# Kernel optimization log

Hardware: AMD Instinct MI355X
Metric: run time of the kernel (lower is better)

## Reference

```python
import jax, jax.numpy as jnp
import numpy as np

TEXT_H = 4096
VISION_H = 1024
SPATIAL_SCALE = 4
DIM = VISION_H * SPATIAL_SCALE  # 4096
B, S, P = 2, 4096, 1024


def setup_inputs() -> dict:
    key = jax.random.key(0)
    ks = jax.random.split(key, 6)
    x = jax.random.normal(ks[0], (B, S, TEXT_H), dtype=jnp.float32)
    total_mask = jax.random.randint(ks[1], (B, S), 0, 2).astype(bool)
    prefix_mask = jnp.ones((B, P), dtype=bool)
    # MLP params: Linear(text->text), GELU, Linear(text->vision*scale)
    W1 = jax.random.normal(ks[2], (TEXT_H, TEXT_H), dtype=jnp.float32) / np.sqrt(TEXT_H)
    b1 = jnp.zeros((TEXT_H,), dtype=jnp.float32)
    W2 = jax.random.normal(ks[3], (TEXT_H, DIM), dtype=jnp.float32) / np.sqrt(TEXT_H)
    b2 = jnp.zeros((DIM,), dtype=jnp.float32)
    return {"x": x, "total_mask": total_mask, "prefix_mask": prefix_mask,
            "W1": W1, "b1": b1, "W2": W2, "b2": b2}


def reference(x, total_mask, prefix_mask, W1, b1, W2, b2):
    # out = zeros; out[total_mask] = mlp(x[total_mask])
    # Equivalent dense form (jit-friendly, same math on every output element):
    h = jax.nn.gelu(jnp.einsum('bst,th->bsh', x, W1) + b1, approximate=False)
    y = jnp.einsum('bsh,hd->bsd', h, W2) + b2          # [B, S, DIM]
    out = jnp.where(total_mask[:, :, None], y, jnp.zeros((), dtype=y.dtype))
    out = out.reshape(out.shape[0], -1, VISION_H)      # [B, S*SCALE, VISION_H]
    prefix_len = prefix_mask.shape[1] * SPATIAL_SCALE  # use_perceiver == False path
    return out[:, prefix_len:]                         # [B, S*SCALE - prefix_len, VISION_H]
```

## Files before the change

kernel.cpp:

```cpp
#include <hip/hip_runtime.h>
#include <hip/hip_bf16.h>
#include <cstdint>
#include <cstddef>

#define TEXT_H_   4096
#define S_TOK     4096
#define P_TOK     1024
#define ROWS_PB   3072
#define M_ROWS    6144
#define NK        4096
#define BK        64
#define NT        (NK / BK)

#define BM0       256
#define BN        256
#define NWGC      384
#define SLOT0_BYTES (64 * 1024)
#define LDS0_TOTAL  (2 * SLOT0_BYTES)

typedef __attribute__((ext_vector_type(8))) short  bf16x8_t;
typedef __attribute__((ext_vector_type(4))) float  f32x4_t;
typedef __attribute__((ext_vector_type(4))) float  fl4_t;
typedef __attribute__((ext_vector_type(4))) ushort u16x4_t;
typedef __attribute__((ext_vector_type(8))) ushort u16x8_t;

__device__ int g_meff;
__device__ int g_rowmap[M_ROWS];

__device__ __forceinline__ ushort f2bf(float f) {
  uint32_t u = __float_as_uint(f);
  u += 0x7FFFu + ((u >> 16) & 1u);
  return (ushort)(u >> 16);
}

__device__ __forceinline__ void gload_lds16(const void* g, void* l) {
  __builtin_amdgcn_global_load_lds((const __attribute__((address_space(1))) void*)g,
                                   (__attribute__((address_space(3))) void*)l, 16, 0, 0);
}

#define BARRIER()    asm volatile("s_barrier" ::: "memory")
#define WAIT_LGKM(n) asm volatile("s_waitcnt lgkmcnt(" #n ")" ::: "memory")
#define WAIT_VM(n)   asm volatile("s_waitcnt vmcnt(" #n ")" ::: "memory")

__global__ void scan_mask_kernel(const void* __restrict__ mask) {
  __shared__ int cnt[1024];
  const int t = threadIdx.x;
  const unsigned* mw = (const unsigned*)mask;
  int isbool = 0;
  for (int i = 0; i < 64; ++i)
    if (mw[i] & ~1u) isbool = 1;
  int pred[6]; int c = 0;
#pragma unroll
  for (int j = 0; j < 6; ++j) {
    const int m  = t * 6 + j;
    const int bb = (m >= ROWS_PB) ? 1 : 0;
    const int idx = bb * S_TOK + P_TOK + (m - bb * ROWS_PB);
    const int v = isbool ? (int)((const unsigned char*)mask)[idx]
                         : ((const int*)mask)[idx];
    pred[j] = (v != 0);
    c += pred[j];
  }
  cnt[t] = c;
  __syncthreads();
  for (int off = 1; off < 1024; off <<= 1) {
    const int v = (t >= off) ? cnt[t - off] : 0;
    __syncthreads();
    cnt[t] += v;
    __syncthreads();
  }
  int p = cnt[t] - c;
  if (t == 1023) g_meff = cnt[1023];
#pragma unroll
  for (int j = 0; j < 6; ++j) {
    const int m = t * 6 + j;
    if (pred[j]) g_rowmap[p++] = m;
  }
}

__global__ void convert_xc_kernel(const float* __restrict__ x, ushort* __restrict__ A1) {
  const int i = blockIdx.x;
  if (i >= g_meff) return;
  const int m  = g_rowmap[i];
  const int bb = (m >= ROWS_PB) ? 1 : 0;
  const int s  = P_TOK + (m - bb * ROWS_PB);
  const float* src = x + ((size_t)bb * S_TOK + s) * TEXT_H_;
  ushort* dst = A1 + (size_t)i * TEXT_H_;
  const int t = threadIdx.x;
#pragma unroll
  for (int c = 0; c < 2; ++c) {
    const int base = t * 16 + c * 8;
    fl4_t f0 = *(const fl4_t*)(src + base);
    fl4_t f1 = *(const fl4_t*)(src + base + 4);
    u16x8_t o;
    o[0] = f2bf(f0[0]); o[1] = f2bf(f0[1]); o[2] = f2bf(f0[2]); o[3] = f2bf(f0[3]);
    o[4] = f2bf(f1[0]); o[5] = f2bf(f1[1]); o[6] = f2bf(f1[2]); o[7] = f2bf(f1[3]);
    *(u16x8_t*)(dst + base) = o;
  }
}

__global__ void transpose_w_kernel(const float* __restrict__ W, ushort* __restrict__ WT) {
  __shared__ float tile[64][65];
  const int kb = blockIdx.x * 64;
  const int nb = blockIdx.y * 64;
  const int t  = threadIdx.x;
  const int lr = t >> 4;
  const int lc = (t & 15) * 4;
#pragma unroll
  for (int it = 0; it < 4; ++it) {
    const int row = lr + it * 16;
    fl4_t v = *(const fl4_t*)(W + (size_t)(kb + row) * NK + nb + lc);
    tile[row][lc + 0] = v[0]; tile[row][lc + 1] = v[1];
    tile[row][lc + 2] = v[2]; tile[row][lc + 3] = v[3];
  }
  __syncthreads();
#pragma unroll
  for (int it = 0; it < 4; ++it) {
    const int n = lr + it * 16;
    u16x4_t o;
    o[0] = f2bf(tile[lc + 0][n]); o[1] = f2bf(tile[lc + 1][n]);
    o[2] = f2bf(tile[lc + 2][n]); o[3] = f2bf(tile[lc + 3][n]);
    *(u16x4_t*)(WT + (size_t)(nb + n) * NK + kb + lc) = o;
  }
}

template <int J>
__device__ __forceinline__ void stage_g0(const ushort* __restrict__ A,
                                         const ushort* __restrict__ Bt,
                                         int row0, int col0, char* lds,
                                         int tau, int w, int l) {
  char* slot = lds + (tau & 1) * SLOT0_BYTES;
  const int kt = tau * BK;
#pragma unroll
  for (int q = 0; q < 2; ++q) {
    const int cg = q * 8 + w;
    if (J == 0 || J == 3) {
      const int CH = (J == 0 ? 0 : 8) + cg + (cg & 8);
      const ushort* src = A + (size_t)(row0 + (CH >> 1) * 16 + (l & 15)) * NK
                            + kt + (CH & 1) * 32 + (l >> 4) * 8;
      gload_lds16(src, slot + CH * 1024 + l * 16);
    } else {
      const int r = (cg >> 2) * 8 + (cg & 3) + (J == 2 ? 4 : 0);
      const ushort* src = Bt + (size_t)(col0 + (r >> 1) * 16 + (l & 15)) * NK
                             + kt + (r & 1) * 32 + (l >> 4) * 8;
      gload_lds16(src, slot + (32 + r) * 1024 + l * 16);
    }
  }
}

template <int MODE>
__launch_bounds__(512, 2)
__global__ void gemm_c_kernel(const ushort* __restrict__ A, const ushort* __restrict__ Bt,
                              const float* __restrict__ bias,
                              ushort* __restrict__ Hout, float* __restrict__ Yout) {
  extern __shared__ char lds[];
  const int tid = threadIdx.x;
  const int l   = tid & 63;
  const int w   = tid >> 6;
  const int wr  = w >> 2;
  const int wc  = w & 3;

  const int meff = g_meff;
  const int mt   = (meff + BM0 - 1) / BM0;
  const int nact = mt * 16;

  const int orig = blockIdx.x;
  if (orig >= nact) return;
  const int bid  = (orig & 7) * (nact >> 3) + (orig >> 3);
  const int row0 = (bid >> 4) * BM0;
  const int col0 = (bid & 15) * BN;

  f32x4_t acc[8][4] = {};

  stage_g0<0>(A, Bt, row0, col0, lds, 0, w, l);
  stage_g0<1>(A, Bt, row0, col0, lds, 0, w, l);
  stage_g0<2>(A, Bt, row0, col0, lds, 0, w, l);
  stage_g0<3>(A, Bt, row0, col0, lds, 0, w, l);
  stage_g0<0>(A, Bt, row0, col0, lds, 1, w, l);
  stage_g0<1>(A, Bt, row0, col0, lds, 1, w, l);
  stage_g0<2>(A, Bt, row0, col0, lds, 1, w, l);
  WAIT_VM(4);
  BARRIER();

  bf16x8_t afL[4][2], bfL[2][2], afH[4][2], bfH[2][2];
#pragma unroll
  for (int mi = 0; mi < 4; ++mi)
#pragma unroll
    for (int kk = 0; kk < 2; ++kk)
      afL[mi][kk] = *(const bf16x8_t*)(lds + (2 * (wr * 8 + mi) + kk) * 1024 + l * 16);
#pragma unroll
  for (int ni = 0; ni < 2; ++ni)
#pragma unroll
    for (int kk = 0; kk < 2; ++kk)
      bfL[ni][kk] = *(const bf16x8_t*)(lds + (32 + 2 * (wc * 4 + ni) + kk) * 1024 + l * 16);

  for (int t = 0; t < NT; ++t) {
    char* s  = lds + (t & 1) * SLOT0_BYTES;
    char* sn = lds + ((t + 1) & 1) * SLOT0_BYTES;

#pragma unroll
    for (int ni = 0; ni < 2; ++ni)
#pragma unroll
      for (int kk = 0; kk < 2; ++kk)
        bfH[ni][kk] = *(const bf16x8_t*)(s + (32 + 2 * (wc * 4 + 2 + ni) + kk) * 1024 + l * 16);
    if (t + 1 < NT) stage_g0<3>(A, Bt, row0, col0, lds, t + 1, w, l);
    WAIT_LGKM(4);
    __builtin_amdgcn_s_setprio(1);
#pragma unroll
    for (int mi = 0; mi < 4; ++mi)
#pragma unroll
      for (int ni = 0; ni < 2; ++ni)
#pragma unroll
        for (int kk = 0; kk < 2; ++kk)
          acc[mi][ni] = __builtin_amdgcn_mfma_f32_16x16x32_bf16(afL[mi][kk], bfL[ni][kk],
                                                                acc[mi][ni], 0, 0, 0);
    __builtin_amdgcn_s_setprio(0);
    BARRIER();

#pragma unroll
    for (int mi = 0; mi < 4; ++mi)
#pragma unroll
      for (int kk = 0; kk < 2; ++kk)
        afH[mi][kk] = *(const bf16x8_t*)(s + (2 * (wr * 8 + 4 + mi) + kk) * 1024 + l * 16);
    if (t + 2 < NT) stage_g0<0>(A, Bt, row0, col0, lds, t + 2, w, l);
    WAIT_LGKM(8);
    __builtin_amdgcn_s_setprio(1);
#pragma unroll
    for (int mi = 0; mi < 4; ++mi)
#pragma unroll
      for (int ni = 0; ni < 2; ++ni)
#pragma unroll
        for (int kk = 0; kk < 2; ++kk)
          acc[mi][2 + ni] = __builtin_amdgcn_mfma_f32_16x16x32_bf16(afL[mi][kk], bfH[ni][kk],
                                                                    acc[mi][2 + ni], 0, 0, 0);
    __builtin_amdgcn_s_setprio(0);
    BARRIER();

    if (t + 1 < NT) {
#pragma unroll
      for (int mi = 0; mi < 4; ++mi)
#pragma unroll
        for (int kk = 0; kk < 2; ++kk)
          afL[mi][kk] = *(const bf16x8_t*)(sn + (2 * (wr * 8 + mi) + kk) * 1024 + l * 16);
    }
    if (t + 2 < NT) stage_g0<1>(A, Bt, row0, col0, lds, t + 2, w, l);
    if (t + 1 < NT) { WAIT_LGKM(8); } else { WAIT_LGKM(0); }
    __builtin_amdgcn_s_setprio(1);
#pragma unroll
    for (int mi = 0; mi < 4; ++mi)
#pragma unroll
      for (int ni = 0; ni < 2; ++ni)
#pragma unroll
        for (int kk = 0; kk < 2; ++kk)
          acc[4 + mi][ni] = __builtin_amdgcn_mfma_f32_16x16x32_bf16(afH[mi][kk], bfL[ni][kk],
                                                                    acc[4 + mi][ni], 0, 0, 0);
    __builtin_amdgcn_s_setprio(0);
    BARRIER();

    if (t + 2 < NT) stage_g0<2>(A, Bt, row0, col0, lds, t + 2, w, l);
    if (t >= NT - 2) { WAIT_VM(0); } else { WAIT_VM(4); }
    BARRIER();
    if (t + 1 < NT) {
#pragma unroll
      for (int ni = 0; ni < 2; ++ni)
#pragma unroll
        for (int kk = 0; kk < 2; ++kk)
          bfL[ni][kk] = *(const bf16x8_t*)(sn + (32 + 2 * (wc * 4 + ni) + kk) * 1024 + l * 16);
    }
    __builtin_amdgcn_s_setprio(1);
#pragma unroll
    for (int mi = 0; mi < 4; ++mi)
#pragma unroll
      for (int ni = 0; ni < 2; ++ni)
#pragma unroll
        for (int kk = 0; kk < 2; ++kk)
          acc[4 + mi][2 + ni] = __builtin_amdgcn_mfma_f32_16x16x32_bf16(afH[mi][kk], bfH[ni][kk],
                                                                        acc[4 + mi][2 + ni], 0, 0, 0);
    __builtin_amdgcn_s_setprio(0);
    BARRIER();
  }

#pragma unroll
  for (int mi = 0; mi < 8; ++mi) {
#pragma unroll
    for (int j = 0; j < 4; ++j) {
      const int r = row0 + wr * 128 + mi * 16 + (l >> 4) * 4 + j;
      if (MODE == 0) {
#pragma unroll
        for (int ni = 0; ni < 4; ++ni) {
          const int c = col0 + wc * 64 + ni * 16 + (l & 15);
          float v = acc[mi][ni][j] + bias[c];
          v = 0.5f * v * (1.0f + erff(v * 0.70710678118654752f));
          Hout[(size_t)r * NK + c] = f2bf(v);
        }
      } else {
        if (r < meff) {
          const int orig_row = g_rowmap[r];
          float* dst = Yout + (size_t)orig_row * NK;
#pragma unroll
          for (int ni = 0; ni < 4; ++ni) {
            const int c = col0 + wc * 64 + ni * 16 + (l & 15);
            dst[c] = acc[mi][ni][j] + bias[c];
          }
        }
      }
    }
  }
}

extern "C" void kernel_launch(void* const* d_in, const int* in_sizes, int n_in,
                              void* d_out, int out_size, void* d_ws, size_t ws_size,
                              hipStream_t stream) {
  const float* x     = (const float*)d_in[0];
  const void*  tmask = (const void*)d_in[1];
  const float* W1    = (const float*)d_in[3];
  const float* b1    = (const float*)d_in[4];
  const float* W2    = (const float*)d_in[5];
  const float* b2    = (const float*)d_in[6];
  float* out = (float*)d_out;

  const size_t offA1  = 0;
  const size_t offB1T = offA1  + (size_t)M_ROWS * NK * 2;
  const size_t offB2T = offB1T + (size_t)NK * NK * 2;
  const size_t offH   = offB2T + (size_t)NK * NK * 2;
  const size_t need   = offH   + (size_t)M_ROWS * NK * 2;
  if (ws_size < need) return;

  char* ws = (char*)d_ws;
  ushort* A1  = (ushort*)(ws + offA1);
  ushort* B1T = (ushort*)(ws + offB1T);
  ushort* B2T = (ushort*)(ws + offB2T);
  ushort* H   = (ushort*)(ws + offH);

  hipMemsetAsync(d_out, 0, (size_t)out_size * sizeof(float), stream);
  scan_mask_kernel<<<dim3(1), dim3(1024), 0, stream>>>(tmask);
  convert_xc_kernel<<<dim3(M_ROWS), dim3(256), 0, stream>>>(x, A1);
  transpose_w_kernel<<<dim3(64, 64), dim3(256), 0, stream>>>(W1, B1T);
  transpose_w_kernel<<<dim3(64, 64), dim3(256), 0, stream>>>(W2, B2T);
  gemm_c_kernel<0><<<dim3(NWGC), dim3(512), LDS0_TOTAL, stream>>>(A1, B1T, b1, H, nullptr);
  gemm_c_kernel<1><<<dim3(NWGC), dim3(512), LDS0_TOTAL, stream>>>(H, B2T, b2, nullptr, out);
}
```

Baseline: 357.5 us.

## Load A fragments directly from global into registers, stage only B in LDS

```diff
diff --git a/kernel.cpp b/kernel.cpp
--- a/kernel.cpp
+++ b/kernel.cpp
@@ -15,8 +15,8 @@
 #define BM0       256
 #define BN        256
 #define NWGC      384
-#define SLOT0_BYTES (64 * 1024)
-#define LDS0_TOTAL  (2 * SLOT0_BYTES)
+#define SLOTB     (32 * 1024)
+#define LDSB_TOTAL (2 * SLOTB)
 
 typedef __attribute__((ext_vector_type(8))) short  bf16x8_t;
 typedef __attribute__((ext_vector_type(4))) float  f32x4_t;
@@ -123,27 +123,16 @@
   }
 }
 
-template <int J>
-__device__ __forceinline__ void stage_g0(const ushort* __restrict__ A,
-                                         const ushort* __restrict__ Bt,
-                                         int row0, int col0, char* lds,
-                                         int tau, int w, int l) {
-  char* slot = lds + (tau & 1) * SLOT0_BYTES;
+__device__ __forceinline__ void stage_B(const ushort* __restrict__ Bt, int col0,
+                                        char* lds, int tau, int w, int l) {
+  char* slot = lds + (tau & 1) * SLOTB;
   const int kt = tau * BK;
 #pragma unroll
-  for (int q = 0; q < 2; ++q) {
-    const int cg = q * 8 + w;
-    if (J == 0 || J == 3) {
-      const int CH = (J == 0 ? 0 : 8) + cg + (cg & 8);
-      const ushort* src = A + (size_t)(row0 + (CH >> 1) * 16 + (l & 15)) * NK
-                            + kt + (CH & 1) * 32 + (l >> 4) * 8;
-      gload_lds16(src, slot + CH * 1024 + l * 16);
-    } else {
-      const int r = (cg >> 2) * 8 + (cg & 3) + (J == 2 ? 4 : 0);
-      const ushort* src = Bt + (size_t)(col0 + (r >> 1) * 16 + (l & 15)) * NK
-                             + kt + (r & 1) * 32 + (l >> 4) * 8;
-      gload_lds16(src, slot + (32 + r) * 1024 + l * 16);
-    }
+  for (int q = 0; q < 4; ++q) {
+    const int r = w * 4 + q;
+    const ushort* src = Bt + (size_t)(col0 + (r >> 1) * 16 + (l & 15)) * NK
+                           + kt + (r & 1) * 32 + (l >> 4) * 8;
+    gload_lds16(src, slot + r * 1024 + l * 16);
   }
 }
 
@@ -169,40 +158,42 @@
   const int row0 = (bid >> 4) * BM0;
   const int col0 = (bid & 15) * BN;
 
+  const ushort* ArowL = A + (size_t)(row0 + wr * 128 + (l & 15)) * NK + (l >> 4) * 8;
+  const ushort* ArowH = ArowL + (size_t)64 * NK;
+
   f32x4_t acc[8][4] = {};
-
-  stage_g0<0>(A, Bt, row0, col0, lds, 0, w, l);
-  stage_g0<1>(A, Bt, row0, col0, lds, 0, w, l);
-  stage_g0<2>(A, Bt, row0, col0, lds, 0, w, l);
-  stage_g0<3>(A, Bt, row0, col0, lds, 0, w, l);
-  stage_g0<0>(A, Bt, row0, col0, lds, 1, w, l);
-  stage_g0<1>(A, Bt, row0, col0, lds, 1, w, l);
-  stage_g0<2>(A, Bt, row0, col0, lds, 1, w, l);
-  WAIT_VM(4);
+  bf16x8_t afL[4][2], afH[4][2], bfL[2][2], bfH[2][2];
+
+  stage_B(Bt, col0, lds, 0, w, l);
+#pragma unroll
+  for (int mi = 0; mi < 4; ++mi)
+#pragma unroll
+    for (int kk = 0; kk < 2; ++kk)
+      afL[mi][kk] = *(const bf16x8_t*)(ArowL + (size_t)(mi * 16) * NK + kk * 32);
+  WAIT_VM(0);
   BARRIER();
 
-  bf16x8_t afL[4][2], bfL[2][2], afH[4][2], bfH[2][2];
-#pragma unroll
-  for (int mi = 0; mi < 4; ++mi)
-#pragma unroll
-    for (int kk = 0; kk < 2; ++kk)
-      afL[mi][kk] = *(const bf16x8_t*)(lds + (2 * (wr * 8 + mi) + kk) * 1024 + l * 16);
-#pragma unroll
-  for (int ni = 0; ni < 2; ++ni)
-#pragma unroll
-    for (int kk = 0; kk < 2; ++kk)
-      bfL[ni][kk] = *(const bf16x8_t*)(lds + (32 + 2 * (wc * 4 + ni) + kk) * 1024 + l * 16);
-
   for (int t = 0; t < NT; ++t) {
-    char* s  = lds + (t & 1) * SLOT0_BYTES;
-    char* sn = lds + ((t + 1) & 1) * SLOT0_BYTES;
-
+    char* s = lds + (t & 1) * SLOTB;
+    const int kt = t * BK;
+    const int ktn = kt + BK;
+
+    if (t + 1 < NT) stage_B(Bt, col0, lds, t + 1, w, l);
 #pragma unroll
     for (int ni = 0; ni < 2; ++ni)
 #pragma unroll
       for (int kk = 0; kk < 2; ++kk)
-        bfH[ni][kk] = *(const bf16x8_t*)(s + (32 + 2 * (wc * 4 + 2 + ni) + kk) * 1024 + l * 16);
-    if (t + 1 < NT) stage_g0<3>(A, Bt, row0, col0, lds, t + 1, w, l);
+        bfL[ni][kk] = *(const bf16x8_t*)(s + (2 * (wc * 4 + ni) + kk) * 1024 + l * 16);
+#pragma unroll
+    for (int ni = 0; ni < 2; ++ni)
+#pragma unroll
+      for (int kk = 0; kk < 2; ++kk)
+        bfH[ni][kk] = *(const bf16x8_t*)(s + (2 * (wc * 4 + 2 + ni) + kk) * 1024 + l * 16);
+#pragma unroll
+    for (int mi = 0; mi < 4; ++mi)
+#pragma unroll
+      for (int kk = 0; kk < 2; ++kk)
+        afH[mi][kk] = *(const bf16x8_t*)(ArowH + (size_t)(mi * 16) * NK + kt + kk * 32);
     WAIT_LGKM(4);
     __builtin_amdgcn_s_setprio(1);
 #pragma unroll
@@ -214,15 +205,8 @@
           acc[mi][ni] = __builtin_amdgcn_mfma_f32_16x16x32_bf16(afL[mi][kk], bfL[ni][kk],
                                                                 acc[mi][ni], 0, 0, 0);
     __builtin_amdgcn_s_setprio(0);
-    BARRIER();
-
-#pragma unroll
-    for (int mi = 0; mi < 4; ++mi)
-#pragma unroll
-      for (int kk = 0; kk < 2; ++kk)
-        afH[mi][kk] = *(const bf16x8_t*)(s + (2 * (wr * 8 + 4 + mi) + kk) * 1024 + l * 16);
-    if (t + 2 < NT) stage_g0<0>(A, Bt, row0, col0, lds, t + 2, w, l);
-    WAIT_LGKM(8);
+
+    WAIT_LGKM(0);
     __builtin_amdgcn_s_setprio(1);
 #pragma unroll
     for (int mi = 0; mi < 4; ++mi)
@@ -233,17 +217,14 @@
           acc[mi][2 + ni] = __builtin_amdgcn_mfma_f32_16x16x32_bf16(afL[mi][kk], bfH[ni][kk],
                                                                     acc[mi][2 + ni], 0, 0, 0);
     __builtin_amdgcn_s_setprio(0);
-    BARRIER();
-
     if (t + 1 < NT) {
 #pragma unroll
       for (int mi = 0; mi < 4; ++mi)
 #pragma unroll
         for (int kk = 0; kk < 2; ++kk)
-          afL[mi][kk] = *(const bf16x8_t*)(sn + (2 * (wr * 8 + mi) + kk) * 1024 + l * 16);
+          afL[mi][kk] = *(const bf16x8_t*)(ArowL + (size_t)(mi * 16) * NK + ktn + kk * 32);
     }
-    if (t + 2 < NT) stage_g0<1>(A, Bt, row0, col0, lds, t + 2, w, l);
-    if (t + 1 < NT) { WAIT_LGKM(8); } else { WAIT_LGKM(0); }
+
     __builtin_amdgcn_s_setprio(1);
 #pragma unroll
     for (int mi = 0; mi < 4; ++mi)
@@ -254,18 +235,7 @@
           acc[4 + mi][ni] = __builtin_amdgcn_mfma_f32_16x16x32_bf16(afH[mi][kk], bfL[ni][kk],
                                                                     acc[4 + mi][ni], 0, 0, 0);
     __builtin_amdgcn_s_setprio(0);
-    BARRIER();
-
-    if (t + 2 < NT) stage_g0<2>(A, Bt, row0, col0, lds, t + 2, w, l);
-    if (t >= NT - 2) { WAIT_VM(0); } else { WAIT_VM(4); }
-    BARRIER();
-    if (t + 1 < NT) {
-#pragma unroll
-      for (int ni = 0; ni < 2; ++ni)
-#pragma unroll
-        for (int kk = 0; kk < 2; ++kk)
-          bfL[ni][kk] = *(const bf16x8_t*)(sn + (32 + 2 * (wc * 4 + ni) + kk) * 1024 + l * 16);
-    }
+
     __builtin_amdgcn_s_setprio(1);
 #pragma unroll
     for (int mi = 0; mi < 4; ++mi)
@@ -276,6 +246,7 @@
           acc[4 + mi][2 + ni] = __builtin_amdgcn_mfma_f32_16x16x32_bf16(afH[mi][kk], bfH[ni][kk],
                                                                         acc[4 + mi][2 + ni], 0, 0, 0);
     __builtin_amdgcn_s_setprio(0);
+    WAIT_VM(0);
     BARRIER();
   }
 
@@ -336,6 +307,6 @@
   convert_xc_kernel<<<dim3(M_ROWS), dim3(256), 0, stream>>>(x, A1);
   transpose_w_kernel<<<dim3(64, 64), dim3(256), 0, stream>>>(W1, B1T);
   transpose_w_kernel<<<dim3(64, 64), dim3(256), 0, stream>>>(W2, B2T);
-  gemm_c_kernel<0><<<dim3(NWGC), dim3(512), LDS0_TOTAL, stream>>>(A1, B1T, b1, H, nullptr);
-  gemm_c_kernel<1><<<dim3(NWGC), dim3(512), LDS0_TOTAL, stream>>>(H, B2T, b2, nullptr, out);
-}
+  gemm_c_kernel<0><<<dim3(NWGC), dim3(512), LDSB_TOTAL, stream>>>(A1, B1T, b1, H, nullptr);
+  gemm_c_kernel<1><<<dim3(NWGC), dim3(512), LDSB_TOTAL, stream>>>(H, B2T, b2, nullptr, out);
+}
```

Result: slower. 724.4 us (+102.6%).

## Fuse prep kernels, zero only masked rows, overlap W2 transpose with GEMM1

Applied to the files above, without the earlier changes.

```diff
diff --git a/kernel.cpp b/kernel.cpp
--- a/kernel.cpp
+++ b/kernel.cpp
@@ -15,6 +15,7 @@
 #define BM0       256
 #define BN        256
 #define NWGC      384
+#define TW2_BLKS  64
 #define SLOT0_BYTES (64 * 1024)
 #define LDS0_TOTAL  (2 * SLOT0_BYTES)
 
@@ -26,6 +27,7 @@
 
 __device__ int g_meff;
 __device__ int g_rowmap[M_ROWS];
+__device__ int g_slot[M_ROWS];
 
 __device__ __forceinline__ ushort f2bf(float f) {
   uint32_t u = __float_as_uint(f);
@@ -73,53 +75,62 @@
 #pragma unroll
   for (int j = 0; j < 6; ++j) {
     const int m = t * 6 + j;
-    if (pred[j]) g_rowmap[p++] = m;
-  }
-}
-
-__global__ void convert_xc_kernel(const float* __restrict__ x, ushort* __restrict__ A1) {
-  const int i = blockIdx.x;
-  if (i >= g_meff) return;
-  const int m  = g_rowmap[i];
-  const int bb = (m >= ROWS_PB) ? 1 : 0;
-  const int s  = P_TOK + (m - bb * ROWS_PB);
-  const float* src = x + ((size_t)bb * S_TOK + s) * TEXT_H_;
-  ushort* dst = A1 + (size_t)i * TEXT_H_;
-  const int t = threadIdx.x;
-#pragma unroll
-  for (int c = 0; c < 2; ++c) {
-    const int base = t * 16 + c * 8;
-    fl4_t f0 = *(const fl4_t*)(src + base);
-    fl4_t f1 = *(const fl4_t*)(src + base + 4);
-    u16x8_t o;
-    o[0] = f2bf(f0[0]); o[1] = f2bf(f0[1]); o[2] = f2bf(f0[2]); o[3] = f2bf(f0[3]);
-    o[4] = f2bf(f1[0]); o[5] = f2bf(f1[1]); o[6] = f2bf(f1[2]); o[7] = f2bf(f1[3]);
-    *(u16x8_t*)(dst + base) = o;
-  }
-}
-
-__global__ void transpose_w_kernel(const float* __restrict__ W, ushort* __restrict__ WT) {
+    if (pred[j]) { g_rowmap[p] = m; g_slot[m] = p; ++p; }
+    else         { g_slot[m] = -1; }
+  }
+}
+
+__global__ void prepass_kernel(const float* __restrict__ x, ushort* __restrict__ A1,
+                               const float* __restrict__ W1, ushort* __restrict__ W1T,
+                               float* __restrict__ out) {
   __shared__ float tile[64][65];
-  const int kb = blockIdx.x * 64;
-  const int nb = blockIdx.y * 64;
-  const int t  = threadIdx.x;
-  const int lr = t >> 4;
-  const int lc = (t & 15) * 4;
-#pragma unroll
-  for (int it = 0; it < 4; ++it) {
-    const int row = lr + it * 16;
-    fl4_t v = *(const fl4_t*)(W + (size_t)(kb + row) * NK + nb + lc);
-    tile[row][lc + 0] = v[0]; tile[row][lc + 1] = v[1];
-    tile[row][lc + 2] = v[2]; tile[row][lc + 3] = v[3];
-  }
-  __syncthreads();
-#pragma unroll
-  for (int it = 0; it < 4; ++it) {
-    const int n = lr + it * 16;
-    u16x4_t o;
-    o[0] = f2bf(tile[lc + 0][n]); o[1] = f2bf(tile[lc + 1][n]);
-    o[2] = f2bf(tile[lc + 2][n]); o[3] = f2bf(tile[lc + 3][n]);
-    *(u16x4_t*)(WT + (size_t)(nb + n) * NK + kb + lc) = o;
+  const int bid = blockIdx.x;
+  const int t   = threadIdx.x;
+  if (bid < M_ROWS) {
+    const int slot = g_slot[bid];
+    if (slot >= 0) {
+      const int bb = (bid >= ROWS_PB) ? 1 : 0;
+      const int s  = P_TOK + (bid - bb * ROWS_PB);
+      const float* src = x + ((size_t)bb * S_TOK + s) * TEXT_H_;
+      ushort* dst = A1 + (size_t)slot * TEXT_H_;
+#pragma unroll
+      for (int c = 0; c < 2; ++c) {
+        const int base = t * 16 + c * 8;
+        fl4_t f0 = *(const fl4_t*)(src + base);
+        fl4_t f1 = *(const fl4_t*)(src + base + 4);
+        u16x8_t o;
+        o[0] = f2bf(f0[0]); o[1] = f2bf(f0[1]); o[2] = f2bf(f0[2]); o[3] = f2bf(f0[3]);
+        o[4] = f2bf(f1[0]); o[5] = f2bf(f1[1]); o[6] = f2bf(f1[2]); o[7] = f2bf(f1[3]);
+        *(u16x8_t*)(dst + base) = o;
+      }
+    } else {
+      float* dst = out + (size_t)bid * NK + t * 16;
+      const fl4_t z = {0.0f, 0.0f, 0.0f, 0.0f};
+#pragma unroll
+      for (int c = 0; c < 4; ++c) *(fl4_t*)(dst + c * 4) = z;
+    }
+  } else {
+    const int tb = bid - M_ROWS;
+    const int kb = (tb & 63) * 64;
+    const int nb = (tb >> 6) * 64;
+    const int lr = t >> 4;
+    const int lc = (t & 15) * 4;
+#pragma unroll
+    for (int it = 0; it < 4; ++it) {
+      const int row = lr + it * 16;
+      fl4_t v = *(const fl4_t*)(W1 + (size_t)(kb + row) * NK + nb + lc);
+      tile[row][lc + 0] = v[0]; tile[row][lc + 1] = v[1];
+      tile[row][lc + 2] = v[2]; tile[row][lc + 3] = v[3];
+    }
+    __syncthreads();
+#pragma unroll
+    for (int it = 0; it < 4; ++it) {
+      const int n = lr + it * 16;
+      u16x4_t o;
+      o[0] = f2bf(tile[lc + 0][n]); o[1] = f2bf(tile[lc + 1][n]);
+      o[2] = f2bf(tile[lc + 2][n]); o[3] = f2bf(tile[lc + 3][n]);
+      *(u16x4_t*)(W1T + (size_t)(nb + n) * NK + kb + lc) = o;
+    }
   }
 }
 
@@ -151,9 +162,45 @@
 __launch_bounds__(512, 2)
 __global__ void gemm_c_kernel(const ushort* __restrict__ A, const ushort* __restrict__ Bt,
                               const float* __restrict__ bias,
+                              const float* __restrict__ Wsrc, ushort* __restrict__ Wdst,
                               ushort* __restrict__ Hout, float* __restrict__ Yout) {
   extern __shared__ char lds[];
   const int tid = threadIdx.x;
+
+  const int orig = blockIdx.x;
+  if (MODE == 0 && orig >= NWGC) {
+    const int tw = orig - NWGC;
+    float (*tile)[65] = (float(*)[65])lds;
+    const int nb = tw * 64;
+    const int lr = tid >> 4;
+    const int lc = (tid & 15) * 4;
+    for (int i = 0; i < 64; ++i) {
+      const int kb = i * 64;
+      if (tid < 256) {
+#pragma unroll
+        for (int it = 0; it < 4; ++it) {
+          const int row = lr + it * 16;
+          fl4_t v = *(const fl4_t*)(Wsrc + (size_t)(kb + row) * NK + nb + lc);
+          tile[row][lc + 0] = v[0]; tile[row][lc + 1] = v[1];
+          tile[row][lc + 2] = v[2]; tile[row][lc + 3] = v[3];
+        }
+      }
+      __syncthreads();
+      if (tid < 256) {
+#pragma unroll
+        for (int it = 0; it < 4; ++it) {
+          const int n = lr + it * 16;
+          u16x4_t o;
+          o[0] = f2bf(tile[lc + 0][n]); o[1] = f2bf(tile[lc + 1][n]);
+          o[2] = f2bf(tile[lc + 2][n]); o[3] = f2bf(tile[lc + 3][n]);
+          *(u16x4_t*)(Wdst + (size_t)(nb + n) * NK + kb + lc) = o;
+        }
+      }
+      __syncthreads();
+    }
+    return;
+  }
+
   const int l   = tid & 63;
   const int w   = tid >> 6;
   const int wr  = w >> 2;
@@ -163,7 +210,6 @@
   const int mt   = (meff + BM0 - 1) / BM0;
   const int nact = mt * 16;
 
-  const int orig = blockIdx.x;
   if (orig >= nact) return;
   const int bid  = (orig & 7) * (nact >> 3) + (orig >> 3);
   const int row0 = (bid >> 4) * BM0;
@@ -331,11 +377,10 @@
   ushort* B2T = (ushort*)(ws + offB2T);
   ushort* H   = (ushort*)(ws + offH);
 
-  hipMemsetAsync(d_out, 0, (size_t)out_size * sizeof(float), stream);
   scan_mask_kernel<<<dim3(1), dim3(1024), 0, stream>>>(tmask);
-  convert_xc_kernel<<<dim3(M_ROWS), dim3(256), 0, stream>>>(x, A1);
-  transpose_w_kernel<<<dim3(64, 64), dim3(256), 0, stream>>>(W1, B1T);
-  transpose_w_kernel<<<dim3(64, 64), dim3(256), 0, stream>>>(W2, B2T);
-  gemm_c_kernel<0><<<dim3(NWGC), dim3(512), LDS0_TOTAL, stream>>>(A1, B1T, b1, H, nullptr);
-  gemm_c_kernel<1><<<dim3(NWGC), dim3(512), LDS0_TOTAL, stream>>>(H, B2T, b2, nullptr, out);
-}
+  prepass_kernel<<<dim3(M_ROWS + 4096), dim3(256), 0, stream>>>(x, A1, W1, B1T, out);
+  gemm_c_kernel<0><<<dim3(NWGC + TW2_BLKS), dim3(512), LDS0_TOTAL, stream>>>(
+      A1, B1T, b1, W2, B2T, H, nullptr);
+  gemm_c_kernel<1><<<dim3(NWGC), dim3(512), LDS0_TOTAL, stream>>>(
+      H, B2T, b2, nullptr, nullptr, nullptr, out);
+}
```

Result: faster. 334.4 us, median of 2 (-6.5%).
